# Kernel optimization log

Hardware: AMD Instinct MI355X
Metric: run time of the kernel (lower is better)

## Reference

```python
import jax, jax.numpy as jnp
import numpy as np

NUM_NODES = 1_000_000
H_DIM = 64
OUT_DIM = 32
NUM_RELS = 64
NUM_BASES = 4
N_SRC0 = 400_000
N_DST1 = 100_000
N_DST2 = 20_000
E1 = 600_000
E2 = 300_000


def setup_inputs() -> dict:
    key = jax.random.key(0)
    ks = jax.random.split(key, 16)
    inp = {
        "input_nodes": jax.random.randint(ks[0], (N_SRC0,), 0, NUM_NODES),
        "src1": jax.random.randint(ks[1], (E1,), 0, N_SRC0),
        "dst1": jax.random.randint(ks[2], (E1,), 0, N_DST1),
        "etype1": jax.random.randint(ks[3], (E1,), 0, NUM_RELS),
        "norm1": jax.random.uniform(ks[4], (E1, 1), dtype=jnp.float32),
        "src2": jax.random.randint(ks[5], (E2,), 0, N_DST1),
        "dst2": jax.random.randint(ks[6], (E2,), 0, N_DST2),
        "etype2": jax.random.randint(ks[7], (E2,), 0, NUM_RELS),
        "norm2": jax.random.uniform(ks[8], (E2, 1), dtype=jnp.float32),
        # learned parameters
        "emb": jax.random.normal(ks[9], (NUM_NODES, H_DIM), dtype=jnp.float32),
        "V1": jax.random.normal(ks[10], (NUM_BASES, H_DIM, H_DIM), dtype=jnp.float32) * 0.05,
        "comp1": jax.random.normal(ks[11], (NUM_RELS, NUM_BASES), dtype=jnp.float32) * 0.3,
        "b1": jnp.zeros((H_DIM,), dtype=jnp.float32),
        "V2": jax.random.normal(ks[12], (NUM_BASES, H_DIM, OUT_DIM), dtype=jnp.float32) * 0.05,
        "comp2": jax.random.normal(ks[13], (NUM_RELS, NUM_BASES), dtype=jnp.float32) * 0.3,
        "b2": jnp.zeros((OUT_DIM,), dtype=jnp.float32),
    }
    return inp


def rel_graph_conv(x, src, dst, etype, norm, V, comp, bias, n_dst):
    """Basis-decomposed RelGraphConv (no self-loop): m_e = (x[src_e] @ W_{etype_e}) * norm_e,
    with W_r = sum_b comp[r,b] V[b]; aggregate by sum into dst nodes, then add bias."""
    xe = x[src]                                 # [E, d] gather of source features
    coeff = comp[etype]                         # [E, B] relation coefficients per edge
    y = jnp.einsum('ed,bdo->ebo', xe, V)        # [E, B, o] feature x each basis
    m = jnp.einsum('ebo,eb->eo', y, coeff)      # [E, o] relation-specific message
    m = m * norm                                # per-edge normalization ([E,1] broadcast)
    h = jax.ops.segment_sum(m, dst, num_segments=n_dst)  # scatter-add to dst
    return h + bias


def reference(input_nodes, src1, dst1, etype1, norm1, src2, dst2, etype2, norm2,
              emb, V1, comp1, b1, V2, comp2, b2):
    x = emb[input_nodes]                                           # [N_src0, h]
    h = rel_graph_conv(x, src1, dst1, etype1, norm1, V1, comp1, b1, N_DST1)
    h = jax.nn.relu(h)
    out = rel_graph_conv(h, src2, dst2, etype2, norm2, V2, comp2, b2, N_DST2)
    return out
```

## Files before the change

kernel.cpp:

```cpp
#include <hip/hip_runtime.h>
#include <stdint.h>

#define NUM_NODES 1000000
#define H_DIM 64
#define OUT_DIM 32
#define NUM_RELS 64
#define NUM_BASES 4
#define N_SRC0 400000
#define N_DST1 100000
#define N_DST2 20000
#define E1 600000
#define E2 300000
#define NDST_TOT (N_DST1 + N_DST2)
#define E_TOT (E1 + E2)

typedef __attribute__((ext_vector_type(8))) short bf16x8;
typedef __attribute__((ext_vector_type(4))) float floatx4;

__device__ __forceinline__ unsigned short f2bf(float f){
  union{float f; unsigned u;} v; v.f=f;
  unsigned u=v.u;
  unsigned r=(u + 0x7FFFu + ((u>>16)&1u))>>16;
  return (unsigned short)r;
}
__device__ __forceinline__ float bf2f(unsigned short h){
  union{unsigned u; float f;} v; v.u=((unsigned)h)<<16; return v.f;
}

__global__ void k_init(const float* __restrict__ V1, const float* __restrict__ V2,
                       ushort* __restrict__ Btab1, ushort* __restrict__ Btab2,
                       int* __restrict__ deg){
  int t = blockIdx.x*blockDim.x + threadIdx.x;
  if (t < NDST_TOT) deg[t] = 0;
  if (t < 16384){
    int j = t & 7, lane = (t>>3)&63, kk = (t>>9)&7, nt = t>>12;
    int kdim = kk*32 + (lane>>4)*8 + j;
    int o = nt*16 + (lane&15);
    int k = kdim>>2, b = kdim&3;
    Btab1[t] = f2bf(V1[(b*64 + k)*64 + o]);
  } else if (t < 24576){
    int u = t - 16384;
    int j = u & 7, lane = (u>>3)&63, kk = (u>>9)&7, nt = u>>12;
    int kdim = kk*32 + (lane>>4)*8 + j;
    int o = nt*16 + (lane&15);
    int k = kdim>>2, b = kdim&3;
    Btab2[u] = f2bf(V2[(b*64 + k)*32 + o]);
  }
}

__global__ void k_hist(const int* __restrict__ dst1, const int* __restrict__ dst2,
                       int* __restrict__ deg){
  int t = blockIdx.x*blockDim.x + threadIdx.x;
  if (t < E1) atomicAdd(&deg[dst1[t]], 1);
  else if (t < E_TOT) atomicAdd(&deg[N_DST1 + dst2[t - E1]], 1);
}

__global__ void k_scan_sum(const int* __restrict__ deg, int* __restrict__ bsum, int n){
  __shared__ int lds[256];
  int tid = threadIdx.x;
  int base = blockIdx.x*1024 + tid*4;
  int s = 0;
  #pragma unroll
  for (int j=0;j<4;j++){ int i = base+j; if (i<n) s += deg[i]; }
  lds[tid] = s; __syncthreads();
  for (int off=128; off>0; off>>=1){ if (tid<off) lds[tid] += lds[tid+off]; __syncthreads(); }
  if (tid==0) bsum[blockIdx.x] = lds[0];
}

__global__ void k_scan_bsum(const int* __restrict__ bsum, int* __restrict__ boff, int nb){
  __shared__ int lds[256];
  int tid = threadIdx.x;
  int v = (tid<nb) ? bsum[tid] : 0;
  lds[tid] = v; __syncthreads();
  for (int off=1; off<256; off<<=1){
    int t = (tid>=off) ? lds[tid-off] : 0; __syncthreads();
    lds[tid] += t; __syncthreads();
  }
  if (tid<nb) boff[tid] = lds[tid] - v;
}

__global__ void k_scan_final(const int* __restrict__ deg, const int* __restrict__ boff,
                             int* __restrict__ offs, int* __restrict__ cursor, int n){
  __shared__ int lds[256];
  int tid = threadIdx.x;
  int base = blockIdx.x*1024 + tid*4;
  int a[4]; int s = 0;
  #pragma unroll
  for (int j=0;j<4;j++){ int i = base+j; a[j] = (i<n)?deg[i]:0; s += a[j]; }
  lds[tid] = s; __syncthreads();
  for (int off=1; off<256; off<<=1){
    int t = (tid>=off) ? lds[tid-off] : 0; __syncthreads();
    lds[tid] += t; __syncthreads();
  }
  int run = boff[blockIdx.x] + (lds[tid] - s);
  #pragma unroll
  for (int j=0;j<4;j++){
    int i = base+j;
    if (i<n){
      offs[i] = run; cursor[i] = run;
      run += a[j];
      if (i == n-1) offs[n] = run;
    }
  }
}

__global__ void k_scatter(const int* __restrict__ input_nodes,
                          const int* __restrict__ src1, const int* __restrict__ dst1,
                          const int* __restrict__ ety1, const float* __restrict__ nrm1,
                          const float* __restrict__ comp1,
                          const int* __restrict__ src2, const int* __restrict__ dst2,
                          const int* __restrict__ ety2, const float* __restrict__ nrm2,
                          const float* __restrict__ comp2,
                          int* __restrict__ cursor, int* __restrict__ ssrc,
                          float4* __restrict__ sc){
  int t = blockIdx.x*blockDim.x + threadIdx.x;
  int d, s, et; float nv; const float* comp;
  if (t < E1){
    d = dst1[t]; s = input_nodes[src1[t]]; et = ety1[t]; nv = nrm1[t]; comp = comp1;
  } else if (t < E_TOT){
    int e = t - E1;
    d = N_DST1 + dst2[e]; s = src2[e]; et = ety2[e]; nv = nrm2[e]; comp = comp2;
  } else return;
  int p = atomicAdd(&cursor[d], 1);
  ssrc[p] = s;
  float4 cp = ((const float4*)comp)[et];
  float4 c; c.x = cp.x*nv; c.y = cp.y*nv; c.z = cp.z*nv; c.w = cp.w*nv;
  sc[p] = c;
}


__global__ __launch_bounds__(1024) void k_agg_gemm1(
    const float* __restrict__ emb, const int* __restrict__ offs,
    const int* __restrict__ ssrc, const float4* __restrict__ sc,
    const ushort* __restrict__ Btab, const float* __restrict__ bias,
    ushort* __restrict__ h_bf){
  __shared__ ushort zt[16][264];
  int lane = threadIdx.x & 63;
  int w = threadIdx.x >> 6;
  int mbase = blockIdx.x * 16;
  int d = mbase + w;
  int e0 = __builtin_amdgcn_readfirstlane(offs[d]);
  int e1 = __builtin_amdgcn_readfirstlane(offs[d+1]);
  float a0=0.f, a1=0.f, a2=0.f, a3=0.f;
  for (int e = e0; e < e1; e += 8){
    int idx[8]; float msk[8];
    #pragma unroll
    for (int k=0;k<8;k++){
      int t = e + k;
      idx[k] = (t < e1) ? t : e0;
      msk[k] = (t < e1) ? 1.f : 0.f;
    }
    int s[8]; float4 c[8];
    #pragma unroll
    for (int k=0;k<8;k++){
      s[k] = __builtin_amdgcn_readfirstlane(ssrc[idx[k]]);
      c[k] = sc[idx[k]];
    }
    float x[8];
    #pragma unroll
    for (int k=0;k<8;k++)
      x[k] = emb[(size_t)s[k]*64 + lane] * msk[k];
    #pragma unroll
    for (int k=0;k<8;k++){
      a0 = fmaf(c[k].x, x[k], a0);
      a1 = fmaf(c[k].y, x[k], a1);
      a2 = fmaf(c[k].z, x[k], a2);
      a3 = fmaf(c[k].w, x[k], a3);
    }
  }
  ushort4 o; o.x=f2bf(a0); o.y=f2bf(a1); o.z=f2bf(a2); o.w=f2bf(a3);
  *(ushort4*)&zt[w][lane*4] = o;
  __syncthreads();
  if (w < 4){
    int quad = lane>>4, l15 = lane&15;
    bf16x8 a[8];
    #pragma unroll
    for (int kk=0; kk<8; kk++)
      a[kk] = *(const bf16x8*)&zt[l15][kk*32 + quad*8];
    floatx4 acc = {0.f,0.f,0.f,0.f};
    #pragma unroll
    for (int kk=0; kk<8; kk++){
      bf16x8 b = *((const bf16x8*)(Btab + ((w*8 + kk)*64 + lane)*8));
      acc = __builtin_amdgcn_mfma_f32_16x16x32_bf16(a[kk], b, acc, 0, 0, 0);
    }
    int col = w*16 + l15;
    float bv = bias[col];
    #pragma unroll
    for (int r=0; r<4; r++){
      int row = mbase + quad*4 + r;
      float v = fmaxf(acc[r] + bv, 0.f);
      h_bf[(size_t)row*64 + col] = f2bf(v);
    }
  }
}

__global__ __launch_bounds__(1024) void k_agg_gemm2(
    const ushort* __restrict__ hin, const int* __restrict__ offs,
    const int* __restrict__ ssrc, const float4* __restrict__ sc,
    const ushort* __restrict__ Btab, const float* __restrict__ bias,
    float* __restrict__ out){
  __shared__ ushort zt[16][264];
  int lane = threadIdx.x & 63;
  int w = threadIdx.x >> 6;
  int mbase = blockIdx.x * 16;
  int d = mbase + w;
  int e0 = __builtin_amdgcn_readfirstlane(offs[d]);
  int e1 = __builtin_amdgcn_readfirstlane(offs[d+1]);
  float a0=0.f, a1=0.f, a2=0.f, a3=0.f;
  for (int e = e0; e < e1; e += 8){
    int idx[8]; float msk[8];
    #pragma unroll
    for (int k=0;k<8;k++){
      int t = e + k;
      idx[k] = (t < e1) ? t : e0;
      msk[k] = (t < e1) ? 1.f : 0.f;
    }
    int s[8]; float4 c[8];
    #pragma unroll
    for (int k=0;k<8;k++){
      s[k] = __builtin_amdgcn_readfirstlane(ssrc[idx[k]]);
      c[k] = sc[idx[k]];
    }
    float x[8];
    #pragma unroll
    for (int k=0;k<8;k++)
      x[k] = bf2f(hin[(size_t)s[k]*64 + lane]) * msk[k];
    #pragma unroll
    for (int k=0;k<8;k++){
      a0 = fmaf(c[k].x, x[k], a0);
      a1 = fmaf(c[k].y, x[k], a1);
      a2 = fmaf(c[k].z, x[k], a2);
      a3 = fmaf(c[k].w, x[k], a3);
    }
  }
  ushort4 o; o.x=f2bf(a0); o.y=f2bf(a1); o.z=f2bf(a2); o.w=f2bf(a3);
  *(ushort4*)&zt[w][lane*4] = o;
  __syncthreads();
  if (w < 2){
    int quad = lane>>4, l15 = lane&15;
    bf16x8 a[8];
    #pragma unroll
    for (int kk=0; kk<8; kk++)
      a[kk] = *(const bf16x8*)&zt[l15][kk*32 + quad*8];
    floatx4 acc = {0.f,0.f,0.f,0.f};
    #pragma unroll
    for (int kk=0; kk<8; kk++){
      bf16x8 b = *((const bf16x8*)(Btab + ((w*8 + kk)*64 + lane)*8));
      acc = __builtin_amdgcn_mfma_f32_16x16x32_bf16(a[kk], b, acc, 0, 0, 0);
    }
    int col = w*16 + l15;
    float bv = bias[col];
    #pragma unroll
    for (int r=0; r<4; r++){
      int row = mbase + quad*4 + r;
      out[(size_t)row*32 + col] = acc[r] + bv;
    }
  }
}

extern "C" void kernel_launch(void* const* d_in, const int* in_sizes, int n_in,
                              void* d_out, int out_size, void* d_ws, size_t ws_size,
                              hipStream_t stream){
  const int*   input_nodes = (const int*)  d_in[0];
  const int*   src1  = (const int*)  d_in[1];
  const int*   dst1  = (const int*)  d_in[2];
  const int*   ety1  = (const int*)  d_in[3];
  const float* norm1 = (const float*)d_in[4];
  const int*   src2  = (const int*)  d_in[5];
  const int*   dst2  = (const int*)  d_in[6];
  const int*   ety2  = (const int*)  d_in[7];
  const float* norm2 = (const float*)d_in[8];
  const float* emb   = (const float*)d_in[9];
  const float* V1    = (const float*)d_in[10];
  const float* comp1 = (const float*)d_in[11];
  const float* b1    = (const float*)d_in[12];
  const float* V2    = (const float*)d_in[13];
  const float* comp2 = (const float*)d_in[14];
  const float* b2    = (const float*)d_in[15];
  float* out = (float*)d_out;

  char* p = (char*)d_ws;
  auto alloc = [&](size_t bytes)->char*{
    char* r = p; p += (bytes + 255) & ~(size_t)255; return r;
  };
  ushort* h_bf  = (ushort*)alloc((size_t)N_DST1*64*2);
  ushort* Btab1 = (ushort*)alloc(16384*2);
  ushort* Btab2 = (ushort*)alloc(8192*2);
  int* deg  = (int*)alloc((size_t)NDST_TOT*4);
  int* cur  = (int*)alloc((size_t)NDST_TOT*4);
  int* offs = (int*)alloc((size_t)(NDST_TOT+1)*4);
  int* bs   = (int*)alloc(256*4);
  int* bo   = (int*)alloc(256*4);
  int* ssrc = (int*)alloc((size_t)E_TOT*4);
  float4* sc = (float4*)alloc((size_t)E_TOT*16);

  k_init<<<(NDST_TOT + 255)/256, 256, 0, stream>>>(V1, V2, Btab1, Btab2, deg);
  k_hist<<<(E_TOT + 255)/256, 256, 0, stream>>>(dst1, dst2, deg);
  int nb = (NDST_TOT + 1023)/1024;
  k_scan_sum<<<nb, 256, 0, stream>>>(deg, bs, NDST_TOT);
  k_scan_bsum<<<1, 256, 0, stream>>>(bs, bo, nb);
  k_scan_final<<<nb, 256, 0, stream>>>(deg, bo, offs, cur, NDST_TOT);
  k_scatter<<<(E_TOT + 255)/256, 256, 0, stream>>>(input_nodes,
                                                   src1, dst1, ety1, norm1, comp1,
                                                   src2, dst2, ety2, norm2, comp2,
                                                   cur, ssrc, sc);
  k_agg_gemm1<<<N_DST1/16, 1024, 0, stream>>>(emb, offs, ssrc, sc, Btab1, b1, h_bf);
  k_agg_gemm2<<<N_DST2/16, 1024, 0, stream>>>(h_bf, offs + N_DST1, ssrc, sc, Btab2, b2, out);

  (void)in_sizes; (void)n_in; (void)out_size; (void)ws_size;
}
```

Before: 481.1 us.

## Pack per-edge src/etype/norm into 8-byte metadata and merge scan into one kernel

Replaces the separate 4-byte source index and 16-byte pre-scaled coefficient arrays with one 8-byte record per edge. The record holds the source id (20 bits), the relation type and the raw norm. The aggregation kernels look up the relation coefficients from the small comp table and scale them by norm on the fly. This cuts scatter writes and gather reads per edge at the cost of a few extra multiplies and a cached table lookup. The three-kernel multi-block prefix scan is also collapsed into a single 1024-thread block. That saves launches, but each thread scans a serial chunk of about 118 elements with strided, uncoalesced access.

```diff
diff --git a/kernel.cpp b/kernel.cpp
--- a/kernel.cpp
+++ b/kernel.cpp
@@ -55,83 +55,52 @@
   else if (t < E_TOT) atomicAdd(&deg[N_DST1 + dst2[t - E1]], 1);
 }
 
-__global__ void k_scan_sum(const int* __restrict__ deg, int* __restrict__ bsum, int n){
-  __shared__ int lds[256];
+__global__ __launch_bounds__(1024) void k_scan(const int* __restrict__ deg,
+                                               int* __restrict__ offs,
+                                               int* __restrict__ cursor, int n){
+  __shared__ int lds[1024];
   int tid = threadIdx.x;
-  int base = blockIdx.x*1024 + tid*4;
+  const int chunk = (n + 1023) >> 10;
+  int lo = tid*chunk; if (lo > n) lo = n;
+  int hi = lo + chunk; if (hi > n) hi = n;
   int s = 0;
-  #pragma unroll
-  for (int j=0;j<4;j++){ int i = base+j; if (i<n) s += deg[i]; }
+  for (int i = lo; i < hi; i++) s += deg[i];
   lds[tid] = s; __syncthreads();
-  for (int off=128; off>0; off>>=1){ if (tid<off) lds[tid] += lds[tid+off]; __syncthreads(); }
-  if (tid==0) bsum[blockIdx.x] = lds[0];
-}
-
-__global__ void k_scan_bsum(const int* __restrict__ bsum, int* __restrict__ boff, int nb){
-  __shared__ int lds[256];
-  int tid = threadIdx.x;
-  int v = (tid<nb) ? bsum[tid] : 0;
-  lds[tid] = v; __syncthreads();
-  for (int off=1; off<256; off<<=1){
-    int t = (tid>=off) ? lds[tid-off] : 0; __syncthreads();
+  for (int off = 1; off < 1024; off <<= 1){
+    int t = (tid >= off) ? lds[tid-off] : 0; __syncthreads();
     lds[tid] += t; __syncthreads();
   }
-  if (tid<nb) boff[tid] = lds[tid] - v;
-}
-
-__global__ void k_scan_final(const int* __restrict__ deg, const int* __restrict__ boff,
-                             int* __restrict__ offs, int* __restrict__ cursor, int n){
-  __shared__ int lds[256];
-  int tid = threadIdx.x;
-  int base = blockIdx.x*1024 + tid*4;
-  int a[4]; int s = 0;
-  #pragma unroll
-  for (int j=0;j<4;j++){ int i = base+j; a[j] = (i<n)?deg[i]:0; s += a[j]; }
-  lds[tid] = s; __syncthreads();
-  for (int off=1; off<256; off<<=1){
-    int t = (tid>=off) ? lds[tid-off] : 0; __syncthreads();
-    lds[tid] += t; __syncthreads();
-  }
-  int run = boff[blockIdx.x] + (lds[tid] - s);
-  #pragma unroll
-  for (int j=0;j<4;j++){
-    int i = base+j;
-    if (i<n){
-      offs[i] = run; cursor[i] = run;
-      run += a[j];
-      if (i == n-1) offs[n] = run;
-    }
-  }
+  int run = lds[tid] - s;
+  for (int i = lo; i < hi; i++){
+    offs[i] = run; cursor[i] = run; run += deg[i];
+  }
+  if (lo < n && hi == n) offs[n] = run;
 }
 
 __global__ void k_scatter(const int* __restrict__ input_nodes,
                           const int* __restrict__ src1, const int* __restrict__ dst1,
                           const int* __restrict__ ety1, const float* __restrict__ nrm1,
-                          const float* __restrict__ comp1,
                           const int* __restrict__ src2, const int* __restrict__ dst2,
                           const int* __restrict__ ety2, const float* __restrict__ nrm2,
-                          const float* __restrict__ comp2,
-                          int* __restrict__ cursor, int* __restrict__ ssrc,
-                          float4* __restrict__ sc){
+                          int* __restrict__ cursor, uint2* __restrict__ meta){
   int t = blockIdx.x*blockDim.x + threadIdx.x;
-  int d, s, et; float nv; const float* comp;
+  int d, s, et; float nv;
   if (t < E1){
-    d = dst1[t]; s = input_nodes[src1[t]]; et = ety1[t]; nv = nrm1[t]; comp = comp1;
+    d = dst1[t]; s = input_nodes[src1[t]]; et = ety1[t]; nv = nrm1[t];
   } else if (t < E_TOT){
     int e = t - E1;
-    d = N_DST1 + dst2[e]; s = src2[e]; et = ety2[e]; nv = nrm2[e]; comp = comp2;
+    d = N_DST1 + dst2[e]; s = src2[e]; et = ety2[e]; nv = nrm2[e];
   } else return;
   int p = atomicAdd(&cursor[d], 1);
-  ssrc[p] = s;
-  float4 cp = ((const float4*)comp)[et];
-  float4 c; c.x = cp.x*nv; c.y = cp.y*nv; c.z = cp.z*nv; c.w = cp.w*nv;
-  sc[p] = c;
+  uint2 m; m.x = (unsigned)s | ((unsigned)et << 20);
+  m.y = __float_as_uint(nv);
+  meta[p] = m;
 }
 
 
 __global__ __launch_bounds__(1024) void k_agg_gemm1(
     const float* __restrict__ emb, const int* __restrict__ offs,
-    const int* __restrict__ ssrc, const float4* __restrict__ sc,
+    const uint2* __restrict__ meta, const float4* __restrict__ comp4,
     const ushort* __restrict__ Btab, const float* __restrict__ bias,
     ushort* __restrict__ h_bf){
   __shared__ ushort zt[16][264];
@@ -153,8 +122,12 @@
     int s[8]; float4 c[8];
     #pragma unroll
     for (int k=0;k<8;k++){
-      s[k] = __builtin_amdgcn_readfirstlane(ssrc[idx[k]]);
-      c[k] = sc[idx[k]];
+      uint2 m = meta[idx[k]];
+      unsigned pk = __builtin_amdgcn_readfirstlane(m.x);
+      float nv = __uint_as_float(__builtin_amdgcn_readfirstlane(m.y));
+      s[k] = (int)(pk & 0xFFFFFu);
+      float4 cp = comp4[pk >> 20];
+      c[k].x = cp.x*nv; c[k].y = cp.y*nv; c[k].z = cp.z*nv; c[k].w = cp.w*nv;
     }
     float x[8];
     #pragma unroll
@@ -196,7 +169,7 @@
 
 __global__ __launch_bounds__(1024) void k_agg_gemm2(
     const ushort* __restrict__ hin, const int* __restrict__ offs,
-    const int* __restrict__ ssrc, const float4* __restrict__ sc,
+    const uint2* __restrict__ meta, const float4* __restrict__ comp4,
     const ushort* __restrict__ Btab, const float* __restrict__ bias,
     float* __restrict__ out){
   __shared__ ushort zt[16][264];
@@ -218,8 +191,12 @@
     int s[8]; float4 c[8];
     #pragma unroll
     for (int k=0;k<8;k++){
-      s[k] = __builtin_amdgcn_readfirstlane(ssrc[idx[k]]);
-      c[k] = sc[idx[k]];
+      uint2 m = meta[idx[k]];
+      unsigned pk = __builtin_amdgcn_readfirstlane(m.x);
+      float nv = __uint_as_float(__builtin_amdgcn_readfirstlane(m.y));
+      s[k] = (int)(pk & 0xFFFFFu);
+      float4 cp = comp4[pk >> 20];
+      c[k].x = cp.x*nv; c[k].y = cp.y*nv; c[k].z = cp.z*nv; c[k].w = cp.w*nv;
     }
     float x[8];
     #pragma unroll
@@ -289,23 +266,19 @@
   int* deg  = (int*)alloc((size_t)NDST_TOT*4);
   int* cur  = (int*)alloc((size_t)NDST_TOT*4);
   int* offs = (int*)alloc((size_t)(NDST_TOT+1)*4);
-  int* bs   = (int*)alloc(256*4);
-  int* bo   = (int*)alloc(256*4);
-  int* ssrc = (int*)alloc((size_t)E_TOT*4);
-  float4* sc = (float4*)alloc((size_t)E_TOT*16);
+  uint2* meta = (uint2*)alloc((size_t)E_TOT*8);
 
   k_init<<<(NDST_TOT + 255)/256, 256, 0, stream>>>(V1, V2, Btab1, Btab2, deg);
   k_hist<<<(E_TOT + 255)/256, 256, 0, stream>>>(dst1, dst2, deg);
-  int nb = (NDST_TOT + 1023)/1024;
-  k_scan_sum<<<nb, 256, 0, stream>>>(deg, bs, NDST_TOT);
-  k_scan_bsum<<<1, 256, 0, stream>>>(bs, bo, nb);
-  k_scan_final<<<nb, 256, 0, stream>>>(deg, bo, offs, cur, NDST_TOT);
+  k_scan<<<1, 1024, 0, stream>>>(deg, offs, cur, NDST_TOT);
   k_scatter<<<(E_TOT + 255)/256, 256, 0, stream>>>(input_nodes,
-                                                   src1, dst1, ety1, norm1, comp1,
-                                                   src2, dst2, ety2, norm2, comp2,
-                                                   cur, ssrc, sc);
-  k_agg_gemm1<<<N_DST1/16, 1024, 0, stream>>>(emb, offs, ssrc, sc, Btab1, b1, h_bf);
-  k_agg_gemm2<<<N_DST2/16, 1024, 0, stream>>>(h_bf, offs + N_DST1, ssrc, sc, Btab2, b2, out);
+                                                   src1, dst1, ety1, norm1,
+                                                   src2, dst2, ety2, norm2,
+                                                   cur, meta);
+  k_agg_gemm1<<<N_DST1/16, 1024, 0, stream>>>(emb, offs, meta,
+                                              (const float4*)comp1, Btab1, b1, h_bf);
+  k_agg_gemm2<<<N_DST2/16, 1024, 0, stream>>>(h_bf, offs + N_DST1, meta,
+                                              (const float4*)comp2, Btab2, b2, out);
 
   (void)in_sizes; (void)n_in; (void)out_size; (void)ws_size;
 }
```

Measured after the change: 734.7 us. 1.53x slower.
